# Performance work log

Hardware: AMD Instinct MI355X
Metric: run time of the kernel (lower is better)

## Reference

```python
import jax, jax.numpy as jnp
import numpy as np

N_QUBITS = 4
N_LAYERS = 6
NUM_CLASSES = 10


def _apply_1q(state, gate, wire):
    # state: (B,2,2,2,2); gate: (2,2) shared or (B,2,2) per-sample
    s = jnp.moveaxis(state, wire + 1, -1)
    if gate.ndim == 3:
        s = jnp.einsum('bij,b...j->b...i', gate, s)
    else:
        s = jnp.einsum('ij,b...j->b...i', gate, s)
    return jnp.moveaxis(s, -1, wire + 1)


def _apply_cnot(state, c, t):
    s = jnp.moveaxis(state, (c + 1, t + 1), (-2, -1))
    s = jnp.stack([s[..., 0, :], s[..., 1, ::-1]], axis=-2)
    return jnp.moveaxis(s, (-2, -1), (c + 1, t + 1))


def _rot(phi, theta, omega):
    # PennyLane Rot = RZ(omega) @ RY(theta) @ RZ(phi)
    c, s = jnp.cos(theta / 2), jnp.sin(theta / 2)
    ep = jnp.exp(-0.5j * (phi + omega))
    em = jnp.exp(-0.5j * (phi - omega))
    return jnp.stack([
        jnp.stack([ep * c, -jnp.conj(em) * s]),
        jnp.stack([em * s, jnp.conj(ep) * c]),
    ])


def _quantum_net(angles, q_weights):
    # batched default.qubit statevector simulation, 4 wires
    B = angles.shape[0]
    state = jnp.zeros((B, 2, 2, 2, 2), jnp.complex64).at[:, 0, 0, 0, 0].set(1.0)
    # AngleEmbedding, rotation='Y' (per-sample RY gates)
    for w in range(N_QUBITS):
        a = angles[:, w]
        c, s = jnp.cos(a / 2), jnp.sin(a / 2)
        g = jnp.stack([jnp.stack([c, -s], -1), jnp.stack([s, c], -1)], -2)
        state = _apply_1q(state, g.astype(jnp.complex64), w)
    # StronglyEntanglingLayers: Rot on each wire, then ring of CNOTs with range r
    for l in range(N_LAYERS):
        for w in range(N_QUBITS):
            state = _apply_1q(state, _rot(q_weights[l, w, 0], q_weights[l, w, 1], q_weights[l, w, 2]), w)
        r = l % (N_QUBITS - 1) + 1
        for w in range(N_QUBITS):
            state = _apply_cnot(state, w, (w + r) % N_QUBITS)
    probs = jnp.abs(state) ** 2  # (B,2,2,2,2)
    z = jnp.array([1.0, -1.0], dtype=probs.dtype)
    exps = [jnp.einsum('bijkl,' + 'ijkl'[w] + '->b', probs, z) for w in range(N_QUBITS)]
    return jnp.stack(exps, -1)  # (B,4) expval PauliZ per wire


def setup_inputs() -> dict:
    key = jax.random.key(0)
    ks = jax.random.split(key, 6)
    B = 65536
    x = jax.random.normal(ks[0], (B, 512), jnp.float32)
    W_pre = jax.random.normal(ks[1], (N_QUBITS, 512), jnp.float32) / np.sqrt(512)
    b_pre = jax.random.normal(ks[2], (N_QUBITS,), jnp.float32) * 0.01
    q_weights = 0.01 * jax.random.normal(ks[3], (N_LAYERS, N_QUBITS, 3), jnp.float32)
    W_post = jax.random.normal(ks[4], (NUM_CLASSES, N_QUBITS), jnp.float32) / np.sqrt(N_QUBITS)
    b_post = jax.random.normal(ks[5], (NUM_CLASSES,), jnp.float32) * 0.01
    return {'x': x, 'W_pre': W_pre, 'b_pre': b_pre, 'q_weights': q_weights,
            'W_post': W_post, 'b_post': b_post}


def reference(x, W_pre, b_pre, q_weights, W_post, b_post):
    pre = x @ W_pre.T + b_pre                 # (B,4)
    angles = jnp.tanh(pre) * np.float32(np.pi)
    q_out = _quantum_net(angles, q_weights)   # (B,4)
    return q_out @ W_post.T + b_post          # (B,10)
```

## Files before the change

### kernel.cpp

```cpp
#include <hip/hip_runtime.h>
#include <math.h>

#define K 512
#define K4 128
#define NQ 4
#define NL 6
#define NC 10

#define A_BLOCK 256
#define A_ROWS_PER_WAVE 8
#define A_ROWS_PER_BLOCK 32

__global__ __launch_bounds__(A_BLOCK, 4) void prenet_kernel(
    const float* __restrict__ x,
    const float* __restrict__ W_pre,
    const float* __restrict__ b_pre,
    float* __restrict__ angles)
{
    const int tid  = threadIdx.x;
    const int wave = tid >> 6;
    const int lane = tid & 63;

    const float4* x4 = (const float4*)x;
    const float4* W4 = (const float4*)W_pre;
    const float4 w0a = W4[0 * K4 + lane], w0b = W4[0 * K4 + 64 + lane];
    const float4 w1a = W4[1 * K4 + lane], w1b = W4[1 * K4 + 64 + lane];
    const float4 w2a = W4[2 * K4 + lane], w2b = W4[2 * K4 + 64 + lane];
    const float4 w3a = W4[3 * K4 + lane], w3b = W4[3 * K4 + 64 + lane];
    const float bp = (lane < NQ) ? b_pre[lane] : 0.f;

    const int rowBase = blockIdx.x * A_ROWS_PER_BLOCK + wave * A_ROWS_PER_WAVE;
    const float4* xrow0 = x4 + (size_t)rowBase * K4;
    float4 xa = xrow0[lane];
    float4 xb = xrow0[64 + lane];

    #pragma unroll
    for (int rr = 0; rr < A_ROWS_PER_WAVE; ++rr) {
        float4 na = xa, nb = xb;
        if (rr + 1 < A_ROWS_PER_WAVE) {
            const float4* nx = x4 + (size_t)(rowBase + rr + 1) * K4;
            na = nx[lane];
            nb = nx[64 + lane];
        }

        float acc0 = xa.x * w0a.x + xa.y * w0a.y + xa.z * w0a.z + xa.w * w0a.w
                   + xb.x * w0b.x + xb.y * w0b.y + xb.z * w0b.z + xb.w * w0b.w;
        float acc1 = xa.x * w1a.x + xa.y * w1a.y + xa.z * w1a.z + xa.w * w1a.w
                   + xb.x * w1b.x + xb.y * w1b.y + xb.z * w1b.z + xb.w * w1b.w;
        float acc2 = xa.x * w2a.x + xa.y * w2a.y + xa.z * w2a.z + xa.w * w2a.w
                   + xb.x * w2b.x + xb.y * w2b.y + xb.z * w2b.z + xb.w * w2b.w;
        float acc3 = xa.x * w3a.x + xa.y * w3a.y + xa.z * w3a.z + xa.w * w3a.w
                   + xb.x * w3b.x + xb.y * w3b.y + xb.z * w3b.z + xb.w * w3b.w;

        const bool b0 = (lane & 1);
        float pA = b0 ? acc1 : acc0;
        float qA = b0 ? acc0 : acc1;
        pA += __shfl_xor(qA, 1);
        float pB = b0 ? acc3 : acc2;
        float qB = b0 ? acc2 : acc3;
        pB += __shfl_xor(qB, 1);
        const bool b1 = (lane & 2);
        float p = b1 ? pB : pA;
        float q = b1 ? pA : pB;
        p += __shfl_xor(q, 2);
        p += __shfl_xor(p, 4);
        p += __shfl_xor(p, 8);
        p += __shfl_xor(p, 16);
        p += __shfl_xor(p, 32);

        if (lane < NQ) {
            const float z = p + bp;
            const float e = __expf(2.f * z);
            const float th = 1.f - 2.f / (e + 1.f);
            angles[(size_t)(rowBase + rr) * NQ + lane] =
                th * 3.14159265358979323846f;
        }
        xa = na; xb = nb;
    }
}

#define B_BLOCK 256

__global__ __launch_bounds__(B_BLOCK, 4) void vqc_kernel(
    const float* __restrict__ angles,
    const float* __restrict__ q_weights,
    const float* __restrict__ W_post,
    const float* __restrict__ b_post,
    float* __restrict__ out)
{
    __shared__ float gates[NL * NQ][8];
    __shared__ float Wpost_s[NC * NQ];
    __shared__ float bpost_s[NC];

    const int tid = threadIdx.x;

    if (tid < NL * NQ) {
        const int l = tid >> 2, w = tid & 3;
        const float phi = q_weights[l * 12 + w * 3 + 0];
        const float th  = q_weights[l * 12 + w * 3 + 1];
        const float om  = q_weights[l * 12 + w * 3 + 2];
        const float c  = cosf(0.5f * th), s = sinf(0.5f * th);
        const float hp = 0.5f * (phi + om), hm = 0.5f * (phi - om);
        const float epr = cosf(hp), epi = -sinf(hp);
        const float emr = cosf(hm), emi = -sinf(hm);
        gates[tid][0] =  epr * c;  gates[tid][1] =  epi * c;
        gates[tid][2] = -emr * s;  gates[tid][3] =  emi * s;
        gates[tid][4] =  emr * s;  gates[tid][5] =  emi * s;
        gates[tid][6] =  epr * c;  gates[tid][7] = -epi * c;
    }
    if (tid >= 64 && tid < 64 + NC * NQ) Wpost_s[tid - 64] = W_post[tid - 64];
    if (tid >= 104 && tid < 104 + NC)    bpost_s[tid - 104] = b_post[tid - 104];
    __syncthreads();

    const int r = blockIdx.x * B_BLOCK + tid;
    const float4 a = ((const float4*)angles)[r];

    float c0, s0, c1, s1, c2, s2, c3, s3;
    __sincosf(0.5f * a.x, &s0, &c0);
    __sincosf(0.5f * a.y, &s1, &c1);
    __sincosf(0.5f * a.z, &s2, &c2);
    __sincosf(0.5f * a.w, &s3, &c3);

    float ar[16], ai[16];
    #pragma unroll
    for (int i = 0; i < 16; ++i) {
        ar[i] = ((i & 8) ? s0 : c0) * ((i & 4) ? s1 : c1)
              * ((i & 2) ? s2 : c2) * ((i & 1) ? s3 : c3);
        ai[i] = 0.f;
    }

    #pragma unroll
    for (int l = 0; l < NL; ++l) {
        #pragma unroll
        for (int w = 0; w < NQ; ++w) {
            const float* G = gates[l * 4 + w];
            const float g00r = G[0], g00i = G[1], g01r = G[2], g01i = G[3];
            const float g10r = G[4], g10i = G[5], g11r = G[6], g11i = G[7];
            const int m = 8 >> w;
            #pragma unroll
            for (int i0 = 0; i0 < 16; ++i0) {
                if (i0 & m) continue;
                const int i1 = i0 | m;
                const float A0r = ar[i0], A0i = ai[i0];
                const float A1r = ar[i1], A1i = ai[i1];
                ar[i0] = g00r * A0r - g00i * A0i + g01r * A1r - g01i * A1i;
                ai[i0] = g00r * A0i + g00i * A0r + g01r * A1i + g01i * A1r;
                ar[i1] = g10r * A0r - g10i * A0i + g11r * A1r - g11i * A1i;
                ai[i1] = g10r * A0i + g10i * A0r + g11r * A1i + g11i * A1r;
            }
        }
        const int rshift = l % 3 + 1;
        #pragma unroll
        for (int w = 0; w < NQ; ++w) {
            const int cm = 8 >> w;
            const int tm = 8 >> ((w + rshift) & 3);
            #pragma unroll
            for (int i = 0; i < 16; ++i) {
                if ((i & cm) && !(i & tm)) {
                    const int ii = i | tm;
                    float t;
                    t = ar[i]; ar[i] = ar[ii]; ar[ii] = t;
                    t = ai[i]; ai[i] = ai[ii]; ai[ii] = t;
                }
            }
        }
    }

    float e0 = 0.f, e1 = 0.f, e2 = 0.f, e3 = 0.f;
    #pragma unroll
    for (int i = 0; i < 16; ++i) {
        const float pr = ar[i] * ar[i] + ai[i] * ai[i];
        e0 += (i & 8) ? -pr : pr;
        e1 += (i & 4) ? -pr : pr;
        e2 += (i & 2) ? -pr : pr;
        e3 += (i & 1) ? -pr : pr;
    }

    float o[NC];
    #pragma unroll
    for (int c = 0; c < NC; ++c) {
        o[c] = bpost_s[c]
             + Wpost_s[c * 4 + 0] * e0 + Wpost_s[c * 4 + 1] * e1
             + Wpost_s[c * 4 + 2] * e2 + Wpost_s[c * 4 + 3] * e3;
    }
    float2* orow2 = (float2*)(out + (size_t)r * NC);
    #pragma unroll
    for (int c = 0; c < 5; ++c)
        orow2[c] = make_float2(o[2 * c], o[2 * c + 1]);
}

extern "C" void kernel_launch(void* const* d_in, const int* in_sizes, int n_in,
                              void* d_out, int out_size, void* d_ws, size_t ws_size,
                              hipStream_t stream) {
    const float* x         = (const float*)d_in[0];
    const float* W_pre     = (const float*)d_in[1];
    const float* b_pre     = (const float*)d_in[2];
    const float* q_weights = (const float*)d_in[3];
    const float* W_post    = (const float*)d_in[4];
    const float* b_post    = (const float*)d_in[5];
    float* out    = (float*)d_out;
    float* angles = (float*)d_ws;

    const int B = in_sizes[0] / K;
    dim3 gridA(B / A_ROWS_PER_BLOCK);
    prenet_kernel<<<gridA, A_BLOCK, 0, stream>>>(x, W_pre, b_pre, angles);
    dim3 gridB(B / B_BLOCK);
    vqc_kernel<<<gridB, B_BLOCK, 0, stream>>>(angles, q_weights, W_post, b_post, out);
}
```

Baseline: 211.0 us.

## Replace cross-lane shuffle reduction with DPP plus shared-memory transpose reduction

The prenet kernel now does the first two butterfly steps with DPP quad-permute moves instead of ds_bpermute shuffles. Each lane writes its partial sum to LDS, and after one barrier every thread reduces 16 partials for one (row, wire) pair, so the angles store becomes coalesced. Rows per block double to 64. This removes the long shuffle chain and the store from only 4 active lanes per row. In exchange it adds LDS traffic, a block-wide sync, and fewer blocks.

```diff
diff --git a/kernel.cpp b/kernel.cpp
--- a/kernel.cpp
+++ b/kernel.cpp
@@ -7,9 +7,18 @@
 #define NL 6
 #define NC 10
 
+__device__ __forceinline__ float dpp_xor1(float v) {
+    return __int_as_float(__builtin_amdgcn_mov_dpp(__float_as_int(v), 0xB1, 0xF, 0xF, true));
+}
+__device__ __forceinline__ float dpp_xor2(float v) {
+    return __int_as_float(__builtin_amdgcn_mov_dpp(__float_as_int(v), 0x4E, 0xF, 0xF, true));
+}
+
 #define A_BLOCK 256
-#define A_ROWS_PER_WAVE 8
-#define A_ROWS_PER_BLOCK 32
+#define A_WAVES 4
+#define A_ROWS_PER_WAVE 16
+#define A_ROWS_PER_BLOCK 64
+#define PART_STRIDE 68
 
 __global__ __launch_bounds__(A_BLOCK, 4) void prenet_kernel(
     const float* __restrict__ x,
@@ -17,6 +26,8 @@
     const float* __restrict__ b_pre,
     float* __restrict__ angles)
 {
+    __shared__ float part[A_ROWS_PER_BLOCK * PART_STRIDE];
+
     const int tid  = threadIdx.x;
     const int wave = tid >> 6;
     const int lane = tid & 63;
@@ -27,9 +38,11 @@
     const float4 w1a = W4[1 * K4 + lane], w1b = W4[1 * K4 + 64 + lane];
     const float4 w2a = W4[2 * K4 + lane], w2b = W4[2 * K4 + 64 + lane];
     const float4 w3a = W4[3 * K4 + lane], w3b = W4[3 * K4 + 64 + lane];
-    const float bp = (lane < NQ) ? b_pre[lane] : 0.f;
 
     const int rowBase = blockIdx.x * A_ROWS_PER_BLOCK + wave * A_ROWS_PER_WAVE;
+
+    const int partOff = (lane & 3) * 16 + (lane >> 2);
+
     const float4* xrow0 = x4 + (size_t)rowBase * K4;
     float4 xa = xrow0[lane];
     float4 xb = xrow0[64 + lane];
@@ -55,27 +68,35 @@
         const bool b0 = (lane & 1);
         float pA = b0 ? acc1 : acc0;
         float qA = b0 ? acc0 : acc1;
-        pA += __shfl_xor(qA, 1);
+        pA += dpp_xor1(qA);
         float pB = b0 ? acc3 : acc2;
         float qB = b0 ? acc2 : acc3;
-        pB += __shfl_xor(qB, 1);
+        pB += dpp_xor1(qB);
         const bool b1 = (lane & 2);
         float p = b1 ? pB : pA;
         float q = b1 ? pA : pB;
-        p += __shfl_xor(q, 2);
-        p += __shfl_xor(p, 4);
-        p += __shfl_xor(p, 8);
-        p += __shfl_xor(p, 16);
-        p += __shfl_xor(p, 32);
-
-        if (lane < NQ) {
-            const float z = p + bp;
-            const float e = __expf(2.f * z);
-            const float th = 1.f - 2.f / (e + 1.f);
-            angles[(size_t)(rowBase + rr) * NQ + lane] =
-                th * 3.14159265358979323846f;
-        }
+        p += dpp_xor2(q);
+
+        part[(wave * A_ROWS_PER_WAVE + rr) * PART_STRIDE + partOff] = p;
+
         xa = na; xb = nb;
+    }
+    __syncthreads();
+
+    {
+        const int row  = tid >> 2;
+        const int wire = tid & 3;
+        const float4* seg4 = (const float4*)&part[row * PART_STRIDE + wire * 16];
+        const float4 s0 = seg4[0], s1 = seg4[1], s2 = seg4[2], s3 = seg4[3];
+        const float s = ((s0.x + s0.y) + (s0.z + s0.w))
+                      + ((s1.x + s1.y) + (s1.z + s1.w))
+                      + ((s2.x + s2.y) + (s2.z + s2.w))
+                      + ((s3.x + s3.y) + (s3.z + s3.w));
+        const float z = s + b_pre[wire];
+        const float e = __expf(2.f * z);
+        const float th = 1.f - 2.f / (e + 1.f);
+        angles[(size_t)blockIdx.x * A_ROWS_PER_BLOCK * NQ + tid] =
+            th * 3.14159265358979323846f;
     }
 }
 
```

After: 208.6 us. No clear change (-1.1%).
